# Performance work log

Hardware: AMD Instinct MI355X
Metric: run time of the kernel (lower is better)

## Reference

```python
import jax, jax.numpy as jnp
import numpy as np
import math

D_MODEL = 1024
N_HEADS = 16
HEAD_DIM = D_MODEL // N_HEADS
N_LAYERS = 2
VOCAB = 32000
MAX_T = 2048
HIDDEN = 4 * D_MODEL
TOP_K = 64
LN_EPS = 1e-5


def setup_inputs() -> dict:
    key = jax.random.key(0)
    ks = jax.random.split(key, 20)
    s = 0.02
    B, T = 1, 2048
    inp = {
        "input_ids": jax.random.randint(ks[0], (B, T), 0, VOCAB, dtype=jnp.int32),
        "Wemb": jax.random.normal(ks[1], (VOCAB, D_MODEL), jnp.float32) * s,
        "Wpos": jax.random.normal(ks[2], (MAX_T, D_MODEL), jnp.float32) * s,
        "ln1_g": jnp.ones((N_LAYERS, D_MODEL), jnp.float32),
        "ln1_b": jnp.zeros((N_LAYERS, D_MODEL), jnp.float32),
        "Wq": jax.random.normal(ks[3], (N_LAYERS, D_MODEL, D_MODEL), jnp.float32) * s,
        "Wk": jax.random.normal(ks[4], (N_LAYERS, D_MODEL, D_MODEL), jnp.float32) * s,
        "Wv": jax.random.normal(ks[5], (N_LAYERS, D_MODEL, D_MODEL), jnp.float32) * s,
        "Wo": jax.random.normal(ks[6], (N_LAYERS, D_MODEL, D_MODEL), jnp.float32) * s,
        "ln2_g": jnp.ones((N_LAYERS, D_MODEL), jnp.float32),
        "ln2_b": jnp.zeros((N_LAYERS, D_MODEL), jnp.float32),
        "W1": jax.random.normal(ks[7], (N_LAYERS, D_MODEL, HIDDEN), jnp.float32) * s,
        "b1": jnp.zeros((N_LAYERS, HIDDEN), jnp.float32),
        "W2": jax.random.normal(ks[8], (N_LAYERS, HIDDEN, D_MODEL), jnp.float32) * s,
        "b2": jnp.zeros((N_LAYERS, D_MODEL), jnp.float32),
        "lnf_g": jnp.ones((D_MODEL,), jnp.float32),
        "lnf_b": jnp.zeros((D_MODEL,), jnp.float32),
    }
    return inp


def layer_norm(x, g, b):
    m = x.mean(-1, keepdims=True)
    v = ((x - m) ** 2).mean(-1, keepdims=True)
    return (x - m) * jax.lax.rsqrt(v + LN_EPS) * g + b


def sparsify_last_dim_topk(x, keep_k):
    # keep top-k entries (by magnitude) along last dim, zero the rest
    a = jnp.abs(x)
    thr = jax.lax.top_k(a, keep_k)[0][..., -1:]
    return jnp.where(a >= thr, x, jnp.zeros_like(x))


def sparse_attention(x, Wq, Wk, Wv, Wo):
    B, T, C = x.shape
    k_keep = min(TOP_K, T)
    feat_keep = max(1, math.ceil(HEAD_DIM * k_keep / T))  # feature_keep_from_attention_keep

    def split(h):  # [B,T,C] -> [B,H,T,hd]
        return h.reshape(B, T, N_HEADS, HEAD_DIM).transpose(0, 2, 1, 3)

    q = sparsify_last_dim_topk(split(x @ Wq), feat_keep)
    k = sparsify_last_dim_topk(split(x @ Wk), feat_keep)
    v = sparsify_last_dim_topk(split(x @ Wv), feat_keep)

    scores = jnp.einsum('bhqd,bhkd->bhqk', q, k) / math.sqrt(HEAD_DIM)
    causal = jnp.tril(jnp.ones((T, T), bool))
    scores = jnp.where(causal, scores, -jnp.inf)

    # row-wise top-k then scatter back into a -inf matrix (as torch.topk + scatter_)
    vals, idx = jax.lax.top_k(scores, k_keep)  # [B,H,T,k]
    bi = jnp.arange(B)[:, None, None, None]
    hi = jnp.arange(N_HEADS)[None, :, None, None]
    ti = jnp.arange(T)[None, None, :, None]
    sparse = jnp.full_like(scores, -jnp.inf).at[bi, hi, ti, idx].set(vals)
    attn = jax.nn.softmax(sparse, axis=-1)

    out = jnp.einsum('bhqk,bhkd->bhqd', attn, v)
    out = out.transpose(0, 2, 1, 3).reshape(B, T, C)
    return out @ Wo


def forward(input_ids, Wemb, Wpos, ln1_g, ln1_b, Wq, Wk, Wv, Wo,
            ln2_g, ln2_b, W1, b1, W2, b2, lnf_g, lnf_b):
    B, T = input_ids.shape
    x = Wemb[input_ids] + Wpos[jnp.arange(T)][None, :, :]
    for l in range(N_LAYERS):
        x = x + sparse_attention(layer_norm(x, ln1_g[l], ln1_b[l]), Wq[l], Wk[l], Wv[l], Wo[l])
        h = layer_norm(x, ln2_g[l], ln2_b[l])
        h = jax.nn.gelu(h @ W1[l] + b1[l], approximate=False) @ W2[l] + b2[l]
        x = x + h
    x = layer_norm(x, lnf_g, lnf_b)
    return x @ Wemb.T  # tied lm head


def reference(input_ids, Wemb, Wpos, ln1_g, ln1_b, Wq, Wk, Wv, Wo,
              ln2_g, ln2_b, W1, b1, W2, b2, lnf_g, lnf_b):
    return forward(input_ids, Wemb, Wpos, ln1_g, ln1_b, Wq, Wk, Wv, Wo,
                   ln2_g, ln2_b, W1, b1, W2, b2, lnf_g, lnf_b)
```

## Files before the change

### kernel.cpp

```cpp
#include <hip/hip_runtime.h>
#include <math.h>

#define D_MODEL 1024
#define N_HEADS 16
#define HEAD_DIM 64
#define HIDDEN 4096
#define TMAX 2048

typedef __attribute__((ext_vector_type(8))) short s16x8;
typedef __attribute__((ext_vector_type(4))) float f32x4;

__device__ __forceinline__ float wave_max_f(float v) {
#pragma unroll
  for (int o = 32; o > 0; o >>= 1) v = fmaxf(v, __shfl_xor(v, o));
  return v;
}
__device__ __forceinline__ float wave_sum_f(float v) {
#pragma unroll
  for (int o = 32; o > 0; o >>= 1) v += __shfl_xor(v, o);
  return v;
}
__device__ __forceinline__ unsigned long long wave_max_u64(unsigned long long k) {
#pragma unroll
  for (int o = 32; o > 0; o >>= 1) {
    unsigned long long u = __shfl_xor(k, o);
    if (u > k) k = u;
  }
  return k;
}
__device__ __forceinline__ unsigned ford(float v) {
  unsigned u = __float_as_uint(v);
  return (u & 0x80000000u) ? ~u : (u | 0x80000000u);
}
__device__ __forceinline__ unsigned short f2bf(float f) {
  unsigned u = __float_as_uint(f);
  u += 0x7FFFu + ((u >> 16) & 1u);
  return (unsigned short)(u >> 16);
}
__device__ __forceinline__ float bf2f(unsigned short h) {
  return __uint_as_float((unsigned)h << 16);
}

__device__ __forceinline__ void gload_lds16(const void* g, void* l) {
  __builtin_amdgcn_global_load_lds(
      (const __attribute__((address_space(1))) void*)g,
      (__attribute__((address_space(3))) void*)l, 16, 0, 0);
}

__global__ __launch_bounds__(256) void embed_kernel(const int* __restrict__ ids,
    const float* __restrict__ Wemb, const float* __restrict__ Wpos, float* __restrict__ X) {
  int t = blockIdx.x, tid = threadIdx.x;
  int id = ids[t];
  float4 e = ((const float4*)(Wemb + (size_t)id * D_MODEL))[tid];
  float4 p = ((const float4*)(Wpos + (size_t)t * D_MODEL))[tid];
  e.x += p.x; e.y += p.y; e.z += p.z; e.w += p.w;
  ((float4*)(X + (size_t)t * D_MODEL))[tid] = e;
}

__global__ __launch_bounds__(256) void ln_kernel(const float* __restrict__ X,
    float* __restrict__ Y, unsigned short* __restrict__ Ybh, unsigned short* __restrict__ Ybl,
    const float* __restrict__ g, const float* __restrict__ b) {
  int row = blockIdx.x, tid = threadIdx.x;
  int lane = tid & 63, wid = tid >> 6;
  __shared__ float red[8];
  float4 v = ((const float4*)(X + (size_t)row * D_MODEL))[tid];
  float s = v.x + v.y + v.z + v.w;
  s = wave_sum_f(s);
  if (lane == 0) red[wid] = s;
  __syncthreads();
  float mean = (red[0] + red[1] + red[2] + red[3]) * (1.0f / D_MODEL);
  float dx = v.x - mean, dy = v.y - mean, dz = v.z - mean, dw = v.w - mean;
  float q = dx * dx + dy * dy + dz * dz + dw * dw;
  q = wave_sum_f(q);
  if (lane == 0) red[4 + wid] = q;
  __syncthreads();
  float var = (red[4] + red[5] + red[6] + red[7]) * (1.0f / D_MODEL);
  float rs = rsqrtf(var + 1e-5f);
  float4 gg = ((const float4*)g)[tid], bb = ((const float4*)b)[tid];
  float4 y;
  y.x = dx * rs * gg.x + bb.x;
  y.y = dy * rs * gg.y + bb.y;
  y.z = dz * rs * gg.z + bb.z;
  y.w = dw * rs * gg.w + bb.w;
  if (Y) ((float4*)(Y + (size_t)row * D_MODEL))[tid] = y;
  if (Ybh) {
    ushort4 oh;
    oh.x = f2bf(y.x); oh.y = f2bf(y.y); oh.z = f2bf(y.z); oh.w = f2bf(y.w);
    ((ushort4*)(Ybh + (size_t)row * D_MODEL))[tid] = oh;
    if (Ybl) {
      ushort4 ol;
      ol.x = f2bf(y.x - bf2f(oh.x)); ol.y = f2bf(y.y - bf2f(oh.y));
      ol.z = f2bf(y.z - bf2f(oh.z)); ol.w = f2bf(y.w - bf2f(oh.w));
      ((ushort4*)(Ybl + (size_t)row * D_MODEL))[tid] = ol;
    }
  }
}

__global__ __launch_bounds__(256) void sparsify_kernel(float* __restrict__ X, int nseg, int fk) {
  int seg = blockIdx.x * 4 + (threadIdx.x >> 6);
  if (seg >= nseg) return;
  int lane = threadIdx.x & 63;
  size_t idx = (size_t)seg * 64 + lane;
  float x = X[idx];
  float a = fabsf(x);
  float cur = INFINITY;
  int remaining = fk;
  float thr = 0.0f;
  for (;;) {
    float cand = (a < cur) ? a : -INFINITY;
    float mv = wave_max_f(cand);
    if (mv == -INFINITY) { thr = mv; break; }
    int c = __popcll(__ballot(a == mv));
    if (c >= remaining) { thr = mv; break; }
    remaining -= c; cur = mv;
  }
  if (!(a >= thr)) X[idx] = 0.0f;
}

__global__ __launch_bounds__(256) void transpose_kernel(const float* __restrict__ in,
    float* __restrict__ out, int R, int Cc) {
  __shared__ float tile[32][33];
  int c0 = blockIdx.x * 32, r0 = blockIdx.y * 32;
  int tx = threadIdx.x & 31, ty = threadIdx.x >> 5;
  for (int i = ty; i < 32; i += 8)
    tile[i][tx] = in[(size_t)(r0 + i) * Cc + c0 + tx];
  __syncthreads();
  for (int i = ty; i < 32; i += 8)
    out[(size_t)(c0 + i) * R + r0 + tx] = tile[tx][i];
}

__global__ __launch_bounds__(256) void transpose_conv_pair_kernel(const float* __restrict__ in,
    unsigned short* __restrict__ oh, unsigned short* __restrict__ ol, int R, int Cc) {
  __shared__ float tile[32][33];
  int c0 = blockIdx.x * 32, r0 = blockIdx.y * 32;
  int tx = threadIdx.x & 31, ty = threadIdx.x >> 5;
  for (int i = ty; i < 32; i += 8)
    tile[i][tx] = in[(size_t)(r0 + i) * Cc + c0 + tx];
  __syncthreads();
  for (int i = ty; i < 32; i += 8) {
    float v = tile[tx][i];
    unsigned short h = f2bf(v);
    size_t idx = (size_t)(c0 + i) * R + r0 + tx;
    oh[idx] = h;
    ol[idx] = f2bf(v - bf2f(h));
  }
}

__global__ __launch_bounds__(256) void conv_bf16_kernel(const float* __restrict__ in,
    unsigned short* __restrict__ out, size_t n) {
  size_t i = ((size_t)blockIdx.x * 256 + threadIdx.x) * 4;
  size_t stride = (size_t)gridDim.x * 1024;
  for (; i < n; i += stride) {
    float4 v = *(const float4*)(in + i);
    ushort4 o;
    o.x = f2bf(v.x); o.y = f2bf(v.y); o.z = f2bf(v.z); o.w = f2bf(v.w);
    *(ushort4*)(out + i) = o;
  }
}

__global__ __launch_bounds__(64) void attn_kernel(const float* __restrict__ Q,
    const float* __restrict__ Kt, const float* __restrict__ V,
    float* __restrict__ Of, unsigned short* __restrict__ Oh, unsigned short* __restrict__ Ol,
    int T) {
  int t = blockIdx.x % T;
  int h = blockIdx.x / T;
  int lane = threadIdx.x;
  unsigned long long lmlt = (1ull << lane) - 1ull;

  __shared__ float sc[TMAX];
  __shared__ float qval[HEAD_DIM];
  __shared__ int qdim[HEAD_DIM];
  constexpr int PCAP = 320;
  __shared__ float posv[PCAP];
  __shared__ int posi[PCAP];
  __shared__ int seli[64];
  __shared__ float selv[64];
  __shared__ float wsel[64];

  int hoff = h * HEAD_DIM;
  float qv = Q[(size_t)t * D_MODEL + hoff + lane];
  unsigned long long nzm = __ballot(qv != 0.0f);
  int nq = __popcll(nzm);
  if (qv != 0.0f) {
    int p = __popcll(nzm & lmlt);
    qval[p] = qv; qdim[p] = lane;
  }
  seli[lane] = 0;
  __syncthreads();

  int Vn = t + 1;
  if (nq == 2) {
    float qA = qval[0], qB = qval[1];
    const float* ktA = Kt + (size_t)(hoff + qdim[0]) * T;
    const float* ktB = Kt + (size_t)(hoff + qdim[1]) * T;
    for (int s = lane; s < Vn; s += 64)
      sc[s] = fmaf(qB, ktB[s], qA * ktA[s]) * 0.125f;
  } else {
    for (int s = lane; s < Vn; s += 64) {
      float acc = 0.0f;
      for (int j = 0; j < nq; ++j)
        acc += qval[j] * Kt[(size_t)(hoff + qdim[j]) * T + s];
      sc[s] = acc * 0.125f;
    }
  }
  __syncthreads();

  int nsel = 0;
  if (Vn <= 64) {
    nsel = Vn;
    if (lane < Vn) { seli[lane] = lane; selv[lane] = sc[lane]; }
    __syncthreads();
  } else {
    int base = 0;
    for (int s0 = 0; s0 < Vn; s0 += 64) {
      int s = s0 + lane;
      float v = (s < Vn) ? sc[s] : -1.0f;
      unsigned long long pm = __ballot(v > 0.0f);
      if (v > 0.0f) {
        int p = base + __popcll(pm & lmlt);
        if (p < PCAP) { posv[p] = v; posi[p] = s; }
      }
      base += __popcll(pm);
    }
    int P = base;
    __syncthreads();

    bool fullpath = false;
    if (P >= 64) {
      if (P <= 128) {
        unsigned long long key0, key1;
        {
          int e0 = lane, e1 = lane + 64;
          key0 = (e0 < P) ? (((unsigned long long)ford(posv[e0]) << 32) |
                             (unsigned long long)(0xFFFFFFFFu - (unsigned)e0)) : 0ull;
          key1 = (e1 < P) ? (((unsigned long long)ford(posv[e1]) << 32) |
                             (unsigned long long)(0xFFFFFFFFu - (unsigned)e1)) : 0ull;
        }
        for (int k = 2; k <= 128; k <<= 1) {
          for (int j = k >> 1; j > 0; j >>= 1) {
            if (j == 64) {
              if (key0 < key1) { unsigned long long tm = key0; key0 = key1; key1 = tm; }
            } else {
              bool iLower = (lane & j) == 0;
              {
                unsigned long long prt = __shfl_xor(key0, j);
                bool desc = ((lane & k) == 0);
                bool keepMax = (iLower == desc);
                key0 = keepMax ? (key0 > prt ? key0 : prt) : (key0 < prt ? key0 : prt);
              }
              {
                unsigned long long prt = __shfl_xor(key1, j);
                int e1 = lane + 64;
                bool desc = ((e1 & k) == 0);
                bool keepMax = (iLower == desc);
                key1 = keepMax ? (key1 > prt ? key1 : prt) : (key1 < prt ? key1 : prt);
              }
            }
          }
        }
        int e = (int)(0xFFFFFFFFu - (unsigned)(key0 & 0xFFFFFFFFull));
        seli[lane] = posi[e];
        selv[lane] = posv[e];
        nsel = 64;
        __syncthreads();
      } else if (P <= PCAP) {
        for (int r = 0; r < 64; ++r) {
          unsigned long long best = 0ull;
          for (int j = lane; j < P; j += 64) {
            float v = posv[j];
            if (v > 0.0f) {
              unsigned long long key =
                  ((unsigned long long)ford(v) << 32) | (unsigned)(0xFFFFFFFFu - (unsigned)j);
              if (key > best) best = key;
            }
          }
          best = wave_max_u64(best);
          int j = (int)(0xFFFFFFFFu - (unsigned)(best & 0xFFFFFFFFull));
          if (lane == (j & 63)) {
            seli[r] = posi[j]; selv[r] = posv[j]; posv[j] = -INFINITY;
          }
          __syncthreads();
        }
        nsel = 64;
      } else {
        fullpath = true;
      }
    } else {
      if (lane < P) { seli[lane] = posi[lane]; selv[lane] = posv[lane]; }
      int need = 64 - P;
      int zbase = 0;
      bool done = false;
      for (int s0 = 0; s0 < Vn && !done; s0 += 64) {
        int s = s0 + lane;
        bool isz = (s < Vn) && (sc[s] == 0.0f);
        unsigned long long zm = __ballot(isz);
        int pre = __popcll(zm & lmlt);
        if (isz && (zbase + pre) < need) {
          seli[P + zbase + pre] = s;
          selv[P + zbase + pre] = 0.0f;
        }
        zbase += __popcll(zm);
        if (zbase >= need) done = true;
      }
      if (zbase >= need) {
        nsel = 64;
        __syncthreads();
      } else {
        fullpath = true;
      }
    }

    if (fullpath) {
      __syncthreads();
      nsel = 64;
      for (int r = 0; r < 64; ++r) {
        unsigned long long best = 0ull;
        for (int s = lane; s < Vn; s += 64) {
          float v = sc[s];
          if (v != -INFINITY) {
            unsigned long long key =
                ((unsigned long long)ford(v) << 32) | (unsigned)(0x7FFFFFFFu - (unsigned)s);
            if (key > best) best = key;
          }
        }
        best = wave_max_u64(best);
        if (best == 0ull) { nsel = r; break; }
        int s = (int)(0x7FFFFFFFu - (unsigned)(best & 0xFFFFFFFFull));
        if (lane == (s & 63)) {
          seli[r] = s; selv[r] = sc[s]; sc[s] = -INFINITY;
        }
        __syncthreads();
      }
    }
  }

  float v = (lane < nsel) ? selv[lane] : -INFINITY;
  float m = wave_max_f(v);
  float w = (lane < nsel) ? expf(v - m) : 0.0f;
  float ds = wave_sum_f(w);
  wsel[lane] = w / ds;
  __syncthreads();

  float o = 0.0f;
#pragma unroll 4
  for (int r = 0; r < 64; ++r)
    o = fmaf(wsel[r], V[(size_t)seli[r] * D_MODEL + hoff + lane], o);

  size_t oidx = (size_t)t * D_MODEL + hoff + lane;
  if (Of) Of[oidx] = o;
  if (Oh) {
    unsigned short hh = f2bf(o);
    Oh[oidx] = hh;
    Ol[oidx] = f2bf(o - bf2f(hh));
  }
}

template <int FLAGS, typename CT, bool SWAPXY = false>
__global__ __launch_bounds__(256) void gemm_bt_bf16(const unsigned short* __restrict__ A,
    const unsigned short* __restrict__ B, CT* __restrict__ C,
    const float* __restrict__ bias, const float* __restrict__ res, int M, int N, int K) {
  constexpr bool HAS_BIAS = (FLAGS & 1) != 0;
  constexpr bool HAS_GELU = (FLAGS & 2) != 0;
  constexpr bool HAS_RES = (FLAGS & 4) != 0;
  __shared__ unsigned short As[128 * 32];
  __shared__ unsigned short Bs[128 * 32];
  int tid = threadIdx.x;
  int lane = tid & 63, wid = tid >> 6;
  int wr = wid >> 1, wc = wid & 1;
  int m0 = (SWAPXY ? blockIdx.x : blockIdx.y) * 128;
  int n0 = (SWAPXY ? blockIdx.y : blockIdx.x) * 128;

  int r_in = lane >> 2;
  int slot = lane & 3;

  f32x4 acc[4][4] = {};

  int fr = lane & 15;
  int ksl = lane >> 4;

  for (int k0 = 0; k0 < K; k0 += 32) {
#pragma unroll
    for (int s = 0; s < 2; ++s) {
      int row = wid * 32 + s * 16 + r_in;
      int ksw = (slot ^ ((row >> 1) & 3)) * 8;
      const unsigned short* ga = A + (size_t)(m0 + row) * K + k0 + ksw;
      const unsigned short* gb = B + (size_t)(n0 + row) * K + k0 + ksw;
      gload_lds16(ga, &As[(wid * 32 + s * 16) * 32]);
      gload_lds16(gb, &Bs[(wid * 32 + s * 16) * 32]);
    }
    asm volatile("s_waitcnt vmcnt(0)" ::: "memory");
    __syncthreads();

    s16x8 av[4], bv[4];
#pragma unroll
    for (int mi = 0; mi < 4; ++mi) {
      int ar = wr * 64 + mi * 16 + fr;
      av[mi] = *(const s16x8*)&As[ar * 32 + ((ksl ^ ((ar >> 1) & 3)) * 8)];
    }
#pragma unroll
    for (int ni = 0; ni < 4; ++ni) {
      int br = wc * 64 + ni * 16 + fr;
      bv[ni] = *(const s16x8*)&Bs[br * 32 + ((ksl ^ ((br >> 1) & 3)) * 8)];
    }
#pragma unroll
    for (int mi = 0; mi < 4; ++mi)
#pragma unroll
      for (int ni = 0; ni < 4; ++ni)
        acc[mi][ni] = __builtin_amdgcn_mfma_f32_16x16x32_bf16(av[mi], bv[ni], acc[mi][ni], 0, 0, 0);
    __syncthreads();
  }

  int cr = lane >> 4, cc = lane & 15;
#pragma unroll
  for (int mi = 0; mi < 4; ++mi) {
#pragma unroll
    for (int j = 0; j < 4; ++j) {
      int row = m0 + wr * 64 + mi * 16 + cr * 4 + j;
#pragma unroll
      for (int ni = 0; ni < 4; ++ni) {
        int col = n0 + wc * 64 + ni * 16 + cc;
        float vv = acc[mi][ni][j];
        if (HAS_BIAS) vv += bias[col];
        if (HAS_GELU) vv = 0.5f * vv * (1.0f + erff(vv * 0.70710678118654752f));
        if (HAS_RES) vv += res[(size_t)row * N + col];
        if constexpr (sizeof(CT) == 2)
          C[(size_t)row * N + col] = (CT)f2bf(vv);
        else
          C[(size_t)row * N + col] = (CT)vv;
      }
    }
  }
}

template <int FLAGS, int OUTMODE>
__global__ __launch_bounds__(256) void gemm3_bt(
    const unsigned short* __restrict__ Ah, const unsigned short* __restrict__ Al,
    const unsigned short* __restrict__ Bh, const unsigned short* __restrict__ Bl,
    float* __restrict__ Cf, unsigned short* __restrict__ Ch, unsigned short* __restrict__ Cl,
    const float* __restrict__ bias, const float* __restrict__ res, int M, int N, int K) {
  constexpr bool HAS_BIAS = (FLAGS & 1) != 0;
  constexpr bool HAS_GELU = (FLAGS & 2) != 0;
  constexpr bool HAS_RES = (FLAGS & 4) != 0;
  __shared__ unsigned short As[2][128 * 32];
  __shared__ unsigned short Bs[2][128 * 32];
  int tid = threadIdx.x;
  int lane = tid & 63, wid = tid >> 6;
  int wr = wid >> 1, wc = wid & 1;
  int m0 = blockIdx.y * 128, n0 = blockIdx.x * 128;

  int r_in = lane >> 2;
  int slot = lane & 3;

  f32x4 acc[4][4] = {};

  int fr = lane & 15;
  int ksl = lane >> 4;

  for (int k0 = 0; k0 < K; k0 += 32) {
#pragma unroll
    for (int s = 0; s < 2; ++s) {
      int row = wid * 32 + s * 16 + r_in;
      int ksw = (slot ^ ((row >> 1) & 3)) * 8;
      size_t ao = (size_t)(m0 + row) * K + k0 + ksw;
      size_t bo = (size_t)(n0 + row) * K + k0 + ksw;
      int ldst = (wid * 32 + s * 16) * 32;
      gload_lds16(Ah + ao, &As[0][ldst]);
      gload_lds16(Al + ao, &As[1][ldst]);
      gload_lds16(Bh + bo, &Bs[0][ldst]);
      gload_lds16(Bl + bo, &Bs[1][ldst]);
    }
    asm volatile("s_waitcnt vmcnt(0)" ::: "memory");
    __syncthreads();

    s16x8 avh[4], avl[4], bvh[4], bvl[4];
#pragma unroll
    for (int mi = 0; mi < 4; ++mi) {
      int ar = wr * 64 + mi * 16 + fr;
      int off = ar * 32 + ((ksl ^ ((ar >> 1) & 3)) * 8);
      avh[mi] = *(const s16x8*)&As[0][off];
      avl[mi] = *(const s16x8*)&As[1][off];
    }
#pragma unroll
    for (int ni = 0; ni < 4; ++ni) {
      int br = wc * 64 + ni * 16 + fr;
      int off = br * 32 + ((ksl ^ ((br >> 1) & 3)) * 8);
      bvh[ni] = *(const s16x8*)&Bs[0][off];
      bvl[ni] = *(const s16x8*)&Bs[1][off];
    }
#pragma unroll
    for (int mi = 0; mi < 4; ++mi)
#pragma unroll
      for (int ni = 0; ni < 4; ++ni) {
        acc[mi][ni] = __builtin_amdgcn_mfma_f32_16x16x32_bf16(avh[mi], bvh[ni], acc[mi][ni], 0, 0, 0);
        acc[mi][ni] = __builtin_amdgcn_mfma_f32_16x16x32_bf16(avl[mi], bvh[ni], acc[mi][ni], 0, 0, 0);
        acc[mi][ni] = __builtin_amdgcn_mfma_f32_16x16x32_bf16(avh[mi], bvl[ni], acc[mi][ni], 0, 0, 0);
      }
    __syncthreads();
  }

  int cr = lane >> 4, cc = lane & 15;
#pragma unroll
  for (int mi = 0; mi < 4; ++mi) {
#pragma unroll
    for (int j = 0; j < 4; ++j) {
      int row = m0 + wr * 64 + mi * 16 + cr * 4 + j;
#pragma unroll
      for (int ni = 0; ni < 4; ++ni) {
        int col = n0 + wc * 64 + ni * 16 + cc;
        float vv = acc[mi][ni][j];
        if (HAS_BIAS) vv += bias[col];
        if (HAS_GELU) vv = 0.5f * vv * (1.0f + erff(vv * 0.70710678118654752f));
        if (HAS_RES) vv += res[(size_t)row * N + col];
        if constexpr (OUTMODE == 0) {
          Cf[(size_t)row * N + col] = vv;
        } else {
          unsigned short h = f2bf(vv);
          Ch[(size_t)row * N + col] = h;
          Cl[(size_t)row * N + col] = f2bf(vv - bf2f(h));
        }
      }
    }
  }
}

__global__ __launch_bounds__(256) void gemm_nn_qkv(const float* __restrict__ A,
    const float* __restrict__ Bq, const float* __restrict__ Bk, const float* __restrict__ Bv,
    float* __restrict__ C, int M, int K) {
  __shared__ float As[16][68];
  __shared__ float Bs[16][68];
  int tid = threadIdx.x;
  int m0 = blockIdx.y * 64;
  int n0g = blockIdx.x * 64;
  const float* B = (n0g < 1024) ? Bq : (n0g < 2048 ? Bk : Bv);
  float* Cb = C + (size_t)(n0g >> 10) * ((size_t)M * 1024);
  int n0 = n0g & 1023;
  int tx = tid & 15, ty = tid >> 4;
  int am = tid >> 2, ak = (tid & 3) * 4;
  int bk = tid >> 4, bn = (tid & 15) * 4;
  const float* Ap = A + (size_t)(m0 + am) * K + ak;
  const float* Bp = B + (size_t)bk * 1024 + n0 + bn;
  float acc[4][4] = {};
  for (int k0 = 0; k0 < K; k0 += 16) {
    float4 a4 = *(const float4*)(Ap + k0);
    float4 b4 = *(const float4*)(Bp + (size_t)k0 * 1024);
    As[ak + 0][am] = a4.x; As[ak + 1][am] = a4.y;
    As[ak + 2][am] = a4.z; As[ak + 3][am] = a4.w;
    *(float4*)&Bs[bk][bn] = b4;
    __syncthreads();
#pragma unroll
    for (int k = 0; k < 16; ++k) {
      float4 bq = *(const float4*)&Bs[k][tx * 4];
#pragma unroll
      for (int i = 0; i < 4; ++i) {
        float av = As[k][ty * 4 + i];
        acc[i][0] += av * bq.x; acc[i][1] += av * bq.y;
        acc[i][2] += av * bq.z; acc[i][3] += av * bq.w;
      }
    }
    __syncthreads();
  }
#pragma unroll
  for (int i = 0; i < 4; ++i) {
    int row = m0 + ty * 4 + i;
#pragma unroll
    for (int j = 0; j < 4; ++j) {
      int col = n0 + tx * 4 + j;
      Cb[(size_t)row * 1024 + col] = acc[i][j];
    }
  }
}

template <int FLAGS>
__global__ __launch_bounds__(256) void gemm_nn(const float* __restrict__ A,
    const float* __restrict__ B, float* __restrict__ C, const float* __restrict__ bias,
    const float* __restrict__ res, int M, int N, int K) {
  constexpr bool HAS_BIAS = (FLAGS & 1) != 0;
  constexpr bool HAS_GELU = (FLAGS & 2) != 0;
  constexpr bool HAS_RES = (FLAGS & 4) != 0;
  __shared__ float As[16][68];
  __shared__ float Bs[16][68];
  int tid = threadIdx.x;
  int m0 = blockIdx.y * 64, n0 = blockIdx.x * 64;
  int tx = tid & 15, ty = tid >> 4;
  int am = tid >> 2, ak = (tid & 3) * 4;
  int bk = tid >> 4, bn = (tid & 15) * 4;
  const float* Ap = A + (size_t)(m0 + am) * K + ak;
  const float* Bp = B + (size_t)bk * N + n0 + bn;
  float acc[4][4] = {};
  for (int k0 = 0; k0 < K; k0 += 16) {
    float4 a4 = *(const float4*)(Ap + k0);
    float4 b4 = *(const float4*)(Bp + (size_t)k0 * N);
    As[ak + 0][am] = a4.x; As[ak + 1][am] = a4.y;
    As[ak + 2][am] = a4.z; As[ak + 3][am] = a4.w;
    *(float4*)&Bs[bk][bn] = b4;
    __syncthreads();
#pragma unroll
    for (int k = 0; k < 16; ++k) {
      float4 bq = *(const float4*)&Bs[k][tx * 4];
#pragma unroll
      for (int i = 0; i < 4; ++i) {
        float av = As[k][ty * 4 + i];
        acc[i][0] += av * bq.x; acc[i][1] += av * bq.y;
        acc[i][2] += av * bq.z; acc[i][3] += av * bq.w;
      }
    }
    __syncthreads();
  }
#pragma unroll
  for (int i = 0; i < 4; ++i) {
    int row = m0 + ty * 4 + i;
#pragma unroll
    for (int j = 0; j < 4; ++j) {
      int col = n0 + tx * 4 + j;
      float vv = acc[i][j];
      if (HAS_BIAS) vv += bias[col];
      if (HAS_GELU) vv = 0.5f * vv * (1.0f + erff(vv * 0.70710678118654752f));
      if (HAS_RES) vv += res[(size_t)row * N + col];
      C[(size_t)row * N + col] = vv;
    }
  }
}

template <int FLAGS>
__global__ __launch_bounds__(256) void gemm_nt(const float* __restrict__ A,
    const float* __restrict__ B, float* __restrict__ C, const float* __restrict__ bias,
    const float* __restrict__ res, int M, int N, int K) {
  constexpr bool HAS_BIAS = (FLAGS & 1) != 0;
  constexpr bool HAS_GELU = (FLAGS & 2) != 0;
  constexpr bool HAS_RES = (FLAGS & 4) != 0;
  __shared__ float As[16][68];
  __shared__ float Bs[16][68];
  int tid = threadIdx.x;
  int m0 = blockIdx.y * 64, n0 = blockIdx.x * 64;
  int tx = tid & 15, ty = tid >> 4;
  int am = tid >> 2, ak = (tid & 3) * 4;
  int bn2 = tid >> 2, bk2 = (tid & 3) * 4;
  const float* Ap = A + (size_t)(m0 + am) * K + ak;
  const float* Bp = B + (size_t)(n0 + bn2) * K + bk2;
  float acc[4][4] = {};
  for (int k0 = 0; k0 < K; k0 += 16) {
    float4 a4 = *(const float4*)(Ap + k0);
    float4 b4 = *(const float4*)(Bp + k0);
    As[ak + 0][am] = a4.x; As[ak + 1][am] = a4.y;
    As[ak + 2][am] = a4.z; As[ak + 3][am] = a4.w;
    Bs[bk2 + 0][bn2] = b4.x; Bs[bk2 + 1][bn2] = b4.y;
    Bs[bk2 + 2][bn2] = b4.z; Bs[bk2 + 3][bn2] = b4.w;
    __syncthreads();
#pragma unroll
    for (int k = 0; k < 16; ++k) {
      float4 bq = *(const float4*)&Bs[k][tx * 4];
#pragma unroll
      for (int i = 0; i < 4; ++i) {
        float av = As[k][ty * 4 + i];
        acc[i][0] += av * bq.x; acc[i][1] += av * bq.y;
        acc[i][2] += av * bq.z; acc[i][3] += av * bq.w;
      }
    }
    __syncthreads();
  }
#pragma unroll
  for (int i = 0; i < 4; ++i) {
    int row = m0 + ty * 4 + i;
#pragma unroll
    for (int j = 0; j < 4; ++j) {
      int col = n0 + tx * 4 + j;
      float vv = acc[i][j];
      if (HAS_BIAS) vv += bias[col];
      if (HAS_GELU) vv = 0.5f * vv * (1.0f + erff(vv * 0.70710678118654752f));
      if (HAS_RES) vv += res[(size_t)row * N + col];
      C[(size_t)row * N + col] = vv;
    }
  }
}

extern "C" void kernel_launch(void* const* d_in, const int* in_sizes, int n_in,
                              void* d_out, int out_size, void* d_ws, size_t ws_size,
                              hipStream_t stream) {
  const int* ids = (const int*)d_in[0];
  const float* Wemb = (const float*)d_in[1];
  const float* Wpos = (const float*)d_in[2];
  const float* ln1_g = (const float*)d_in[3];
  const float* ln1_b = (const float*)d_in[4];
  const float* Wq = (const float*)d_in[5];
  const float* Wk = (const float*)d_in[6];
  const float* Wv = (const float*)d_in[7];
  const float* Wo = (const float*)d_in[8];
  const float* ln2_g = (const float*)d_in[9];
  const float* ln2_b = (const float*)d_in[10];
  const float* W1 = (const float*)d_in[11];
  const float* b1 = (const float*)d_in[12];
  const float* W2 = (const float*)d_in[13];
  const float* b2 = (const float*)d_in[14];
  const float* lnf_g = (const float*)d_in[15];
  const float* lnf_b = (const float*)d_in[16];

  const int T = in_sizes[0];
  const int D = D_MODEL;
  const int VOC = in_sizes[1] / D;

  char* ws = (char*)d_ws;
  float* x = (float*)(ws);
  float* xn = (float*)(ws + 8388608ull);
  unsigned short* xnbh = (unsigned short*)(ws + 8388608ull);
  unsigned short* xnbl = (unsigned short*)(ws + 12582912ull);
  float* q = (float*)(ws + 16777216ull);
  float* k = (float*)(ws + 25165824ull);
  float* v = (float*)(ws + 33554432ull);
  float* kt = (float*)(ws + 41943040ull);
  unsigned short* w1th = (unsigned short*)(ws + 16777216ull);
  unsigned short* w1tl = (unsigned short*)(ws + 25165824ull);
  unsigned short* w2th = (unsigned short*)(ws + 33554432ull);
  unsigned short* w2tl = (unsigned short*)(ws + 41943040ull);
  unsigned short* hbh = (unsigned short*)(ws + 50331648ull);
  unsigned short* hbl = (unsigned short*)(ws + 67108864ull);
  unsigned short* woth = (unsigned short*)(ws + 83886080ull);
  unsigned short* wotl = (unsigned short*)(ws + 85983232ull);
  unsigned short* wembb = (unsigned short*)(ws + 16777216ull);
  const size_t NEED = 88080384ull;

  int kkeep = (T < 64) ? T : 64;
  int fk = (HEAD_DIM * kkeep + T - 1) / T;
  if (fk < 1) fk = 1;
  int nseg = T * N_HEADS;

  embed_kernel<<<T, 256, 0, stream>>>(ids, Wemb, Wpos, x);

  if (ws_size >= NEED && (T % 128) == 0 && (VOC % 128) == 0 &&
      (size_t)VOC * D * 2 <= 67108864ull) {
    for (int l = 0; l < 2; ++l) {
      const float* wq = Wq + (size_t)l * D * D;
      const float* wk = Wk + (size_t)l * D * D;
      const float* wv = Wv + (size_t)l * D * D;
      const float* wo = Wo + (size_t)l * D * D;

      ln_kernel<<<T, 256, 0, stream>>>(x, xn, nullptr, nullptr,
                                       ln1_g + (size_t)l * D, ln1_b + (size_t)l * D);

      gemm_nn_qkv<<<dim3(3 * D / 64, T / 64), 256, 0, stream>>>(xn, wq, wk, wv, q, T, D);

      sparsify_kernel<<<(3 * nseg + 3) / 4, 256, 0, stream>>>(q, 3 * nseg, fk);

      transpose_kernel<<<dim3(D / 32, T / 32), 256, 0, stream>>>(k, kt, T, D);

      attn_kernel<<<T * N_HEADS, 64, 0, stream>>>(q, kt, v, nullptr, xnbh, xnbl, T);

      transpose_conv_pair_kernel<<<dim3(D / 32, D / 32), 256, 0, stream>>>(wo, woth, wotl, D, D);
      gemm3_bt<4, 0><<<dim3(D / 128, T / 128), 256, 0, stream>>>(
          xnbh, xnbl, woth, wotl, x, nullptr, nullptr, nullptr, x, T, D, D);

      ln_kernel<<<T, 256, 0, stream>>>(x, nullptr, xnbh, xnbl,
                                       ln2_g + (size_t)l * D, ln2_b + (size_t)l * D);

      transpose_conv_pair_kernel<<<dim3(HIDDEN / 32, D / 32), 256, 0, stream>>>(
          W1 + (size_t)l * D * HIDDEN, w1th, w1tl, D, HIDDEN);
      gemm3_bt<3, 1><<<dim3(HIDDEN / 128, T / 128), 256, 0, stream>>>(
          xnbh, xnbl, w1th, w1tl, nullptr, hbh, hbl,
          b1 + (size_t)l * HIDDEN, nullptr, T, HIDDEN, D);
      transpose_conv_pair_kernel<<<dim3(D / 32, HIDDEN / 32), 256, 0, stream>>>(
          W2 + (size_t)l * HIDDEN * D, w2th, w2tl, HIDDEN, D);
      gemm3_bt<5, 0><<<dim3(D / 128, T / 128), 256, 0, stream>>>(
          hbh, hbl, w2th, w2tl, x, nullptr, nullptr,
          b2 + (size_t)l * D, x, T, D, HIDDEN);
    }

    ln_kernel<<<T, 256, 0, stream>>>(x, nullptr, xnbh, nullptr, lnf_g, lnf_b);

    conv_bf16_kernel<<<4096, 256, 0, stream>>>(Wemb, wembb, (size_t)VOC * D);

    gemm_bt_bf16<0, float, true><<<dim3(T / 128, VOC / 128), 256, 0, stream>>>(
        xnbh, wembb, (float*)d_out, nullptr, nullptr, T, VOC, D);
  } else {
    float* hbuf = q;
    for (int l = 0; l < 2; ++l) {
      const float* wq = Wq + (size_t)l * D * D;
      const float* wk = Wk + (size_t)l * D * D;
      const float* wv = Wv + (size_t)l * D * D;
      const float* wo = Wo + (size_t)l * D * D;

      ln_kernel<<<T, 256, 0, stream>>>(x, xn, nullptr, nullptr,
                                       ln1_g + (size_t)l * D, ln1_b + (size_t)l * D);

      dim3 g1(D / 64, T / 64);
      gemm_nn<0><<<g1, 256, 0, stream>>>(xn, wq, q, nullptr, nullptr, T, D, D);
      gemm_nn<0><<<g1, 256, 0, stream>>>(xn, wk, k, nullptr, nullptr, T, D, D);
      gemm_nn<0><<<g1, 256, 0, stream>>>(xn, wv, v, nullptr, nullptr, T, D, D);

      sparsify_kernel<<<(nseg + 3) / 4, 256, 0, stream>>>(q, nseg, fk);
      sparsify_kernel<<<(nseg + 3) / 4, 256, 0, stream>>>(k, nseg, fk);
      sparsify_kernel<<<(nseg + 3) / 4, 256, 0, stream>>>(v, nseg, fk);

      transpose_kernel<<<dim3(D / 32, T / 32), 256, 0, stream>>>(k, kt, T, D);

      attn_kernel<<<T * N_HEADS, 64, 0, stream>>>(q, kt, v, xn, nullptr, nullptr, T);

      gemm_nn<4><<<g1, 256, 0, stream>>>(xn, wo, x, nullptr, x, T, D, D);

      ln_kernel<<<T, 256, 0, stream>>>(x, xn, nullptr, nullptr,
                                       ln2_g + (size_t)l * D, ln2_b + (size_t)l * D);

      gemm_nn<3><<<dim3(HIDDEN / 64, T / 64), 256, 0, stream>>>(
          xn, W1 + (size_t)l * D * HIDDEN, hbuf, b1 + (size_t)l * HIDDEN, nullptr, T, HIDDEN, D);
      gemm_nn<5><<<g1, 256, 0, stream>>>(
          hbuf, W2 + (size_t)l * HIDDEN * D, x, b2 + (size_t)l * D, x, T, D, HIDDEN);
    }

    ln_kernel<<<T, 256, 0, stream>>>(x, xn, nullptr, nullptr, lnf_g, lnf_b);

    gemm_nt<0><<<dim3(VOC / 64, T / 64), 256, 0, stream>>>(
        xn, Wemb, (float*)d_out, nullptr, nullptr, T, VOC, D);
  }
}
```

Baseline: 1.649 ms.

## Move QKV projection to split-bf16 MFMA GEMM and reverse attention block order

Replaces the FP32 SIMT QKV GEMM with a 128x128-tile MFMA kernel that uses hi/lo bf16 splitting (three MFMAs per tile) to keep near-FP32 accuracy. LayerNorm now writes bf16 hi/lo pairs directly, and the Wq/Wk/Wv weights are transposed and converted into workspace on every call. Attention blocks are also launched in reverse token order, likely to schedule the heavier late rows first. The extra transpose/convert launches and the threefold MFMA work add cost in exchange for much higher matrix throughput.

```diff
diff --git a/kernel.cpp b/kernel.cpp
--- a/kernel.cpp
+++ b/kernel.cpp
@@ -162,7 +162,7 @@
     const float* __restrict__ Kt, const float* __restrict__ V,
     float* __restrict__ Of, unsigned short* __restrict__ Oh, unsigned short* __restrict__ Ol,
     int T) {
-  int t = blockIdx.x % T;
+  int t = T - 1 - (blockIdx.x % T);
   int h = blockIdx.x / T;
   int lane = threadIdx.x;
   unsigned long long lmlt = (1ull << lane) - 1ull;
@@ -523,49 +523,86 @@
   }
 }
 
-__global__ __launch_bounds__(256) void gemm_nn_qkv(const float* __restrict__ A,
-    const float* __restrict__ Bq, const float* __restrict__ Bk, const float* __restrict__ Bv,
+__global__ __launch_bounds__(256) void gemm3_qkv(
+    const unsigned short* __restrict__ Ah, const unsigned short* __restrict__ Al,
+    const unsigned short* __restrict__ Bqh, const unsigned short* __restrict__ Bql,
+    const unsigned short* __restrict__ Bkh, const unsigned short* __restrict__ Bkl,
+    const unsigned short* __restrict__ Bvh, const unsigned short* __restrict__ Bvl,
     float* __restrict__ C, int M, int K) {
-  __shared__ float As[16][68];
-  __shared__ float Bs[16][68];
+  __shared__ unsigned short As[2][128 * 32];
+  __shared__ unsigned short Bs[2][128 * 32];
   int tid = threadIdx.x;
-  int m0 = blockIdx.y * 64;
-  int n0g = blockIdx.x * 64;
-  const float* B = (n0g < 1024) ? Bq : (n0g < 2048 ? Bk : Bv);
-  float* Cb = C + (size_t)(n0g >> 10) * ((size_t)M * 1024);
+  int lane = tid & 63, wid = tid >> 6;
+  int wr = wid >> 1, wc = wid & 1;
+  int m0 = blockIdx.y * 128;
+  int n0g = blockIdx.x * 128;
+  int mat = n0g >> 10;
+  const unsigned short* Bh = (mat == 0) ? Bqh : (mat == 1 ? Bkh : Bvh);
+  const unsigned short* Bl = (mat == 0) ? Bql : (mat == 1 ? Bkl : Bvl);
+  float* Cb = C + (size_t)mat * ((size_t)M * 1024);
   int n0 = n0g & 1023;
-  int tx = tid & 15, ty = tid >> 4;
-  int am = tid >> 2, ak = (tid & 3) * 4;
-  int bk = tid >> 4, bn = (tid & 15) * 4;
-  const float* Ap = A + (size_t)(m0 + am) * K + ak;
-  const float* Bp = B + (size_t)bk * 1024 + n0 + bn;
-  float acc[4][4] = {};
-  for (int k0 = 0; k0 < K; k0 += 16) {
-    float4 a4 = *(const float4*)(Ap + k0);
-    float4 b4 = *(const float4*)(Bp + (size_t)k0 * 1024);
-    As[ak + 0][am] = a4.x; As[ak + 1][am] = a4.y;
-    As[ak + 2][am] = a4.z; As[ak + 3][am] = a4.w;
-    *(float4*)&Bs[bk][bn] = b4;
-    __syncthreads();
-#pragma unroll
-    for (int k = 0; k < 16; ++k) {
-      float4 bq = *(const float4*)&Bs[k][tx * 4];
-#pragma unroll
-      for (int i = 0; i < 4; ++i) {
-        float av = As[k][ty * 4 + i];
-        acc[i][0] += av * bq.x; acc[i][1] += av * bq.y;
-        acc[i][2] += av * bq.z; acc[i][3] += av * bq.w;
-      }
-    }
-    __syncthreads();
-  }
-#pragma unroll
-  for (int i = 0; i < 4; ++i) {
-    int row = m0 + ty * 4 + i;
+
+  int r_in = lane >> 2;
+  int slot = lane & 3;
+
+  f32x4 acc[4][4] = {};
+
+  int fr = lane & 15;
+  int ksl = lane >> 4;
+
+  for (int k0 = 0; k0 < K; k0 += 32) {
+#pragma unroll
+    for (int s = 0; s < 2; ++s) {
+      int row = wid * 32 + s * 16 + r_in;
+      int ksw = (slot ^ ((row >> 1) & 3)) * 8;
+      size_t ao = (size_t)(m0 + row) * K + k0 + ksw;
+      size_t bo = (size_t)(n0 + row) * K + k0 + ksw;
+      int ldst = (wid * 32 + s * 16) * 32;
+      gload_lds16(Ah + ao, &As[0][ldst]);
+      gload_lds16(Al + ao, &As[1][ldst]);
+      gload_lds16(Bh + bo, &Bs[0][ldst]);
+      gload_lds16(Bl + bo, &Bs[1][ldst]);
+    }
+    asm volatile("s_waitcnt vmcnt(0)" ::: "memory");
+    __syncthreads();
+
+    s16x8 avh[4], avl[4], bvh[4], bvl[4];
+#pragma unroll
+    for (int mi = 0; mi < 4; ++mi) {
+      int ar = wr * 64 + mi * 16 + fr;
+      int off = ar * 32 + ((ksl ^ ((ar >> 1) & 3)) * 8);
+      avh[mi] = *(const s16x8*)&As[0][off];
+      avl[mi] = *(const s16x8*)&As[1][off];
+    }
+#pragma unroll
+    for (int ni = 0; ni < 4; ++ni) {
+      int br = wc * 64 + ni * 16 + fr;
+      int off = br * 32 + ((ksl ^ ((br >> 1) & 3)) * 8);
+      bvh[ni] = *(const s16x8*)&Bs[0][off];
+      bvl[ni] = *(const s16x8*)&Bs[1][off];
+    }
+#pragma unroll
+    for (int mi = 0; mi < 4; ++mi)
+#pragma unroll
+      for (int ni = 0; ni < 4; ++ni) {
+        acc[mi][ni] = __builtin_amdgcn_mfma_f32_16x16x32_bf16(avh[mi], bvh[ni], acc[mi][ni], 0, 0, 0);
+        acc[mi][ni] = __builtin_amdgcn_mfma_f32_16x16x32_bf16(avl[mi], bvh[ni], acc[mi][ni], 0, 0, 0);
+        acc[mi][ni] = __builtin_amdgcn_mfma_f32_16x16x32_bf16(avh[mi], bvl[ni], acc[mi][ni], 0, 0, 0);
+      }
+    __syncthreads();
+  }
+
+  int cr = lane >> 4, cc = lane & 15;
+#pragma unroll
+  for (int mi = 0; mi < 4; ++mi) {
 #pragma unroll
     for (int j = 0; j < 4; ++j) {
-      int col = n0 + tx * 4 + j;
-      Cb[(size_t)row * 1024 + col] = acc[i][j];
+      int row = m0 + wr * 64 + mi * 16 + cr * 4 + j;
+#pragma unroll
+      for (int ni = 0; ni < 4; ++ni) {
+        int col = n0 + wc * 64 + ni * 16 + cc;
+        Cb[(size_t)row * 1024 + col] = acc[mi][ni][j];
+      }
     }
   }
 }
@@ -713,6 +750,12 @@
   unsigned short* w2tl = (unsigned short*)(ws + 41943040ull);
   unsigned short* hbh = (unsigned short*)(ws + 50331648ull);
   unsigned short* hbl = (unsigned short*)(ws + 67108864ull);
+  unsigned short* wqth = (unsigned short*)(ws + 50331648ull);
+  unsigned short* wqtl = (unsigned short*)(ws + 52428800ull);
+  unsigned short* wkth = (unsigned short*)(ws + 54525952ull);
+  unsigned short* wktl = (unsigned short*)(ws + 56623104ull);
+  unsigned short* wvth = (unsigned short*)(ws + 58720256ull);
+  unsigned short* wvtl = (unsigned short*)(ws + 60817408ull);
   unsigned short* woth = (unsigned short*)(ws + 83886080ull);
   unsigned short* wotl = (unsigned short*)(ws + 85983232ull);
   unsigned short* wembb = (unsigned short*)(ws + 16777216ull);
@@ -733,10 +776,15 @@
       const float* wv = Wv + (size_t)l * D * D;
       const float* wo = Wo + (size_t)l * D * D;
 
-      ln_kernel<<<T, 256, 0, stream>>>(x, xn, nullptr, nullptr,
+      ln_kernel<<<T, 256, 0, stream>>>(x, nullptr, xnbh, xnbl,
                                        ln1_g + (size_t)l * D, ln1_b + (size_t)l * D);
 
-      gemm_nn_qkv<<<dim3(3 * D / 64, T / 64), 256, 0, stream>>>(xn, wq, wk, wv, q, T, D);
+      transpose_conv_pair_kernel<<<dim3(D / 32, D / 32), 256, 0, stream>>>(wq, wqth, wqtl, D, D);
+      transpose_conv_pair_kernel<<<dim3(D / 32, D / 32), 256, 0, stream>>>(wk, wkth, wktl, D, D);
+      transpose_conv_pair_kernel<<<dim3(D / 32, D / 32), 256, 0, stream>>>(wv, wvth, wvtl, D, D);
+
+      gemm3_qkv<<<dim3(3 * D / 128, T / 128), 256, 0, stream>>>(
+          xnbh, xnbl, wqth, wqtl, wkth, wktl, wvth, wvtl, q, T, D);
 
       sparsify_kernel<<<(3 * nseg + 3) / 4, 256, 0, stream>>>(q, 3 * nseg, fk);
 
```

New measurement: 1.428 ms. 13.4% less time.
